# Performance work log

Hardware: AMD Instinct MI355X
Metric: run time of the kernel (lower is better)

Reference implementation:

```python
import jax, jax.numpy as jnp
import numpy as np

N_NODES = 100000
N_EDGES = 1600000
IN_DIM = 128
HEADS = 4
HEAD_DIM = 16  # hidden_dim 64 // 4 heads
HID = HEADS * HEAD_DIM
NEG_SLOPE = 0.2


def setup_inputs() -> dict:
    key = jax.random.key(0)
    ks = jax.random.split(key, 20)
    inp = {
        "x": jax.random.normal(ks[0], (N_NODES, IN_DIM), dtype=jnp.float32),
        "edge_index": jax.random.randint(ks[1], (2, N_EDGES), 0, N_NODES, dtype=jnp.int32),
    }
    dims = [IN_DIM, HID, HID]
    for l in range(3):
        d_in = dims[l]
        sc = 1.0 / np.sqrt(d_in)
        inp[f"w{l}"] = jax.random.normal(ks[2 + 4 * l], (d_in, HID), dtype=jnp.float32) * sc
        inp[f"asrc{l}"] = jax.random.normal(ks[3 + 4 * l], (HEADS, HEAD_DIM), dtype=jnp.float32) * 0.1
        inp[f"adst{l}"] = jax.random.normal(ks[4 + 4 * l], (HEADS, HEAD_DIM), dtype=jnp.float32) * 0.1
        inp[f"b{l}"] = jnp.zeros((HID,), dtype=jnp.float32)
    inp["out_w"] = jax.random.normal(ks[14], (HID, 1), dtype=jnp.float32) * (1.0 / np.sqrt(HID))
    inp["out_b"] = jnp.zeros((1,), dtype=jnp.float32)
    return inp


def _gat_layer(h, src, dst, W, a_src, a_dst, b):
    # h: [N, d_in]; src/dst: [E'] (self-loops already appended)
    n = h.shape[0]
    xh = (h @ W).reshape(n, HEADS, HEAD_DIM)              # [N,H,C]
    al_s = jnp.sum(xh * a_src, axis=-1)                   # [N,H]
    al_d = jnp.sum(xh * a_dst, axis=-1)                   # [N,H]
    e = jax.nn.leaky_relu(al_s[src] + al_d[dst], NEG_SLOPE)  # [E',H]
    # segment-softmax over incoming edges of each destination node
    m = jax.ops.segment_max(e, dst, num_segments=n)       # [N,H]
    p = jnp.exp(e - m[dst])
    z = jax.ops.segment_sum(p, dst, num_segments=n)       # [N,H]
    alpha = p / (z[dst] + 1e-16)                          # [E',H]
    msg = xh[src] * alpha[:, :, None]                     # [E',H,C]
    out = jax.ops.segment_sum(msg, dst, num_segments=n)   # [N,H,C]
    return out.reshape(n, HID) + b


def reference(x, edge_index, w0, asrc0, adst0, b0, w1, asrc1, adst1, b1,
              w2, asrc2, adst2, b2, out_w, out_b):
    n = x.shape[0]
    loops = jnp.arange(n, dtype=edge_index.dtype)
    src = jnp.concatenate([edge_index[0], loops])  # PyG GATConv adds self-loops
    dst = jnp.concatenate([edge_index[1], loops])
    h = x
    params = [(w0, asrc0, adst0, b0), (w1, asrc1, adst1, b1), (w2, asrc2, adst2, b2)]
    for W, a_s, a_d, b in params:
        h = _gat_layer(h, src, dst, W, a_s, a_d, b)
        h = jax.nn.relu(h)
    return (h @ out_w + out_b).squeeze(-1)  # [N]
```

## Files before the change

### kernel.cpp

```cpp
#include <hip/hip_runtime.h>


#define NBMAX 512
#define SCHUNK 4096
#define BCAP 8192
#define PADSLACK 768

typedef __attribute__((ext_vector_type(8))) short bf16x8;
typedef __attribute__((ext_vector_type(4))) float f32x4;

__device__ inline unsigned short bf16_rtn(float x) {
    union { float f; unsigned u; } a; a.f = x;
    return (unsigned short)((a.u + 0x7FFFu + ((a.u >> 16) & 1u)) >> 16);
}
__device__ inline float bf16_to_f(unsigned short s) {
    union { unsigned u; float f; } b; b.u = ((unsigned)s) << 16;
    return b.f;
}

__global__ __launch_bounds__(256) void k_init(int* __restrict__ bhist, int nb,
                                              float* __restrict__ als, float* __restrict__ xh, int n) {
    int i = blockIdx.x * 256 + threadIdx.x;
    if (i < nb) bhist[i] = 0;
    int j = i - NBMAX;
    if (j >= 0 && j < 4) als[(size_t)n * 4 + j] = -1e30f;
    int k = i - NBMAX - 4;
    if (k >= 0 && k < 64) xh[(size_t)n * 64 + k] = 0.f;
}

__global__ __launch_bounds__(256) void k_bhist(const int* __restrict__ dst, int* __restrict__ bhist, int e) {
    __shared__ unsigned int h[NBMAX];
    int t = threadIdx.x;
    h[t] = 0;
    h[t + 256] = 0;
    __syncthreads();
    for (int i = blockIdx.x * 256 + t; i < e; i += gridDim.x * 256)
        atomicAdd(&h[dst[i] >> 8], 1u);
    __syncthreads();
    if (h[t]) atomicAdd(&bhist[t], (int)h[t]);
    if (h[t + 256]) atomicAdd(&bhist[t + 256], (int)h[t + 256]);
}

__global__ __launch_bounds__(512) void k_bscan(const int* __restrict__ bhist, int* __restrict__ boffs,
                                               int* __restrict__ bfill, int nb, int e) {
    __shared__ int s[NBMAX];
    int t = threadIdx.x;
    int v = (t < nb) ? bhist[t] : 0;
    s[t] = v;
    __syncthreads();
    for (int o = 1; o < 512; o <<= 1) {
        int add = (t >= o) ? s[t - o] : 0;
        __syncthreads();
        s[t] += add;
        __syncthreads();
    }
    boffs[t] = s[t] - v;
    if (t == 511) boffs[512] = s[511];
    bfill[t] = 0;
}

__global__ __launch_bounds__(512) void k_bscatter(const int* __restrict__ src, const int* __restrict__ dst,
                                                  const int* __restrict__ boffs, int* __restrict__ bfill,
                                                  unsigned int* __restrict__ edata, int e) {
    __shared__ unsigned int hist[NBMAX];
    __shared__ unsigned int loc[NBMAX];
    __shared__ int gbase[NBMAX];
    __shared__ unsigned int stmp[NBMAX];
    __shared__ unsigned int sortbuf[SCHUNK];
    __shared__ int posbuf[SCHUNK];
    int t = threadIdx.x;
    int i0 = blockIdx.x * SCHUNK;
    int cnt = min(SCHUNK, e - i0);
    hist[t] = 0;
    __syncthreads();
    for (int j = t; j < cnt; j += 512) atomicAdd(&hist[dst[i0 + j] >> 8], 1u);
    __syncthreads();
    unsigned int v = hist[t];
    stmp[t] = v;
    __syncthreads();
    for (int o = 1; o < 512; o <<= 1) {
        unsigned int add = (t >= o) ? stmp[t - o] : 0;
        __syncthreads();
        stmp[t] += add;
        __syncthreads();
    }
    loc[t] = stmp[t] - v;
    int gb = 0;
    if (v > 0) gb = atomicAdd(&bfill[t], (int)v);
    gbase[t] = boffs[t] + gb - (int)loc[t];
    hist[t] = loc[t];
    __syncthreads();
    for (int j = t; j < cnt; j += 512) {
        int d = dst[i0 + j];
        int s = src[i0 + j];
        int b = d >> 8;
        unsigned int p = atomicAdd(&hist[b], 1u);
        sortbuf[p] = (unsigned int)s | ((unsigned int)(d & 255) << 24);
        posbuf[p] = gbase[b] + (int)p;
    }
    __syncthreads();
    for (int j = t; j < cnt; j += 512) edata[posbuf[j]] = sortbuf[j];
}

__global__ __launch_bounds__(256) void k_bfinal(const unsigned int* __restrict__ edata,
                                                const int* __restrict__ boffs, int* __restrict__ poffs,
                                                int* __restrict__ pend, int* __restrict__ ssrc,
                                                int n, int nb) {
    __shared__ unsigned int hist[256];
    __shared__ unsigned int stmp[256];
    __shared__ unsigned int loc[256];
    __shared__ unsigned int cnt_s[256];
    __shared__ unsigned int srcbuf[BCAP];
    int b = blockIdx.x;
    int t = threadIdx.x;
    int e0 = boffs[b], e1 = boffs[b + 1];
    int cnt = e1 - e0;
    int pb = e0 + b * PADSLACK;
    hist[t] = 0;
    __syncthreads();
    for (int j = t; j < cnt; j += 256) atomicAdd(&hist[edata[e0 + j] >> 24], 1u);
    __syncthreads();
    unsigned int v = hist[t];
    unsigned int v4 = (v + 3u) & ~3u;
    cnt_s[t] = v;
    stmp[t] = v4;
    __syncthreads();
    for (int o = 1; o < 256; o <<= 1) {
        unsigned int add = (t >= o) ? stmp[t - o] : 0;
        __syncthreads();
        stmp[t] += add;
        __syncthreads();
    }
    loc[t] = stmp[t] - v4;
    int ptot = (int)stmp[255];
    int node = b * 256 + t;
    if (node < n) {
        poffs[node] = pb + (int)loc[t];
        pend[node] = pb + (int)(loc[t] + v4);
    }
    hist[t] = loc[t];
    __syncthreads();
    if (cnt + PADSLACK <= BCAP) {
        for (int j = t; j < cnt; j += 256) {
            unsigned int p = edata[e0 + j];
            unsigned int pos = atomicAdd(&hist[p >> 24], 1u);
            srcbuf[pos] = p & 0xFFFFFFu;
        }
        for (unsigned int k = v; k < v4; ++k) srcbuf[loc[t] + k] = (unsigned int)n;
        __syncthreads();
        for (int j = t; j < ptot; j += 256) ssrc[pb + j] = (int)srcbuf[j];
    } else {
        for (int j = t; j < cnt; j += 256) {
            unsigned int p = edata[e0 + j];
            unsigned int pos = atomicAdd(&hist[p >> 24], 1u);
            ssrc[pb + (int)pos] = (int)(p & 0xFFFFFFu);
        }
        for (unsigned int k = v; k < v4; ++k) ssrc[pb + (int)(loc[t] + k)] = n;
    }
}

__global__ __launch_bounds__(256) void k_wprep(const float* __restrict__ w0, const float* __restrict__ w1,
                                               const float* __restrict__ w2,
                                               unsigned short* __restrict__ p0h, unsigned short* __restrict__ p0l,
                                               unsigned short* __restrict__ p1h, unsigned short* __restrict__ p1l,
                                               unsigned short* __restrict__ p2h, unsigned short* __restrict__ p2l) {
    int g = blockIdx.x * 256 + threadIdx.x;
    const float* W;
    unsigned short *ph, *pl;
    int idx;
    if (g < 1024) { W = w0; ph = p0h; pl = p0l; idx = g; }
    else if (g < 1536) { W = w1; ph = p1h; pl = p1l; idx = g - 1024; }
    else if (g < 2048) { W = w2; ph = p2h; pl = p2l; idx = g - 1536; }
    else return;
    int ko = idx >> 6, nn = idx & 63;
#pragma unroll
    for (int j = 0; j < 8; ++j) {
        float w = W[(size_t)(ko * 8 + j) * 64 + nn];
        unsigned short hb = bf16_rtn(w);
        ph[(size_t)idx * 8 + j] = hb;
        pl[(size_t)idx * 8 + j] = bf16_rtn(w - bf16_to_f(hb));
    }
}

template <int D_IN>
__global__ __launch_bounds__(256) void k_mgemm(const float* __restrict__ h,
                                               const unsigned short* __restrict__ wph,
                                               const unsigned short* __restrict__ wpl,
                                               const float* __restrict__ asrc, const float* __restrict__ adst,
                                               float* __restrict__ xh, float* __restrict__ als,
                                               float* __restrict__ ald, int n) {
    int t = threadIdx.x;
    int wv = t >> 6, lane = t & 63;
    int quad = lane >> 4, l16 = lane & 15;
    int m0 = blockIdx.x * 64 + wv * 16;
    int node_a = m0 + l16;
    int mm = min(node_a, n - 1);
    const float* hrow = h + (size_t)mm * D_IN + quad * 8;

    f32x4 acc[4];
#pragma unroll
    for (int i = 0; i < 4; ++i) acc[i] = (f32x4){0.f, 0.f, 0.f, 0.f};

    constexpr int KSTEPS = D_IN / 32;
#pragma unroll
    for (int s = 0; s < KSTEPS; ++s) {
        float4 a0 = *(const float4*)(hrow + s * 32);
        float4 a1 = *(const float4*)(hrow + s * 32 + 4);
        float av[8] = {a0.x, a0.y, a0.z, a0.w, a1.x, a1.y, a1.z, a1.w};
        bf16x8 ahi, alo;
#pragma unroll
        for (int j = 0; j < 8; ++j) {
            unsigned short hb = bf16_rtn(av[j]);
            ahi[j] = (short)hb;
            alo[j] = (short)bf16_rtn(av[j] - bf16_to_f(hb));
        }
        const unsigned short* bbase = wph + ((size_t)((s * 4 + quad) * 64 + l16)) * 8;
        const unsigned short* bbasel = wpl + ((size_t)((s * 4 + quad) * 64 + l16)) * 8;
#pragma unroll
        for (int nt = 0; nt < 4; ++nt) {
            bf16x8 bhi = *(const bf16x8*)(bbase + (size_t)nt * 16 * 8);
            bf16x8 blo = *(const bf16x8*)(bbasel + (size_t)nt * 16 * 8);
            acc[nt] = __builtin_amdgcn_mfma_f32_16x16x32_bf16(ahi, bhi, acc[nt], 0, 0, 0);
            acc[nt] = __builtin_amdgcn_mfma_f32_16x16x32_bf16(ahi, blo, acc[nt], 0, 0, 0);
            acc[nt] = __builtin_amdgcn_mfma_f32_16x16x32_bf16(alo, bhi, acc[nt], 0, 0, 0);
        }
    }
#pragma unroll
    for (int nt = 0; nt < 4; ++nt) {
        float as_l = asrc[nt * 16 + l16];
        float ad_l = adst[nt * 16 + l16];
#pragma unroll
        for (int r = 0; r < 4; ++r) {
            int node = m0 + quad * 4 + r;
            float c = acc[nt][r];
            if (node < n) xh[(size_t)node * 64 + nt * 16 + l16] = c;
            float ps = c * as_l, pd = c * ad_l;
            ps += __shfl_xor(ps, 1, 64); pd += __shfl_xor(pd, 1, 64);
            ps += __shfl_xor(ps, 2, 64); pd += __shfl_xor(pd, 2, 64);
            ps += __shfl_xor(ps, 4, 64); pd += __shfl_xor(pd, 4, 64);
            ps += __shfl_xor(ps, 8, 64); pd += __shfl_xor(pd, 8, 64);
            if (l16 == 0 && node < n) {
                als[node * 4 + nt] = ps;
                ald[node * 4 + nt] = pd;
            }
        }
    }
}

__device__ inline float4 lrelu4(float4 v) {
    float4 r;
    r.x = v.x >= 0.f ? v.x : 0.2f * v.x;
    r.y = v.y >= 0.f ? v.y : 0.2f * v.y;
    r.z = v.z >= 0.f ? v.z : 0.2f * v.z;
    r.w = v.w >= 0.f ? v.w : 0.2f * v.w;
    return r;
}

#define ACCUM(LO, HI, ACC, ZS)                                                  \
    {                                                                           \
        int g_ = ((LO) - s0) >> 2, gb_ = ((HI) - s0) >> 2;                      \
        for (; g_ + 4 <= gb_; g_ += 4) {                                        \
            int4 uu0 = *(const int4*)&ub[g_ * 4];                               \
            int4 uu1 = *(const int4*)&ub[g_ * 4 + 4];                           \
            int4 uu2 = *(const int4*)&ub[g_ * 4 + 8];                           \
            int4 uu3 = *(const int4*)&ub[g_ * 4 + 12];                          \
            float4 pp0 = *(const float4*)&per[g_ * 4];                          \
            float4 pp1 = *(const float4*)&per[g_ * 4 + 4];                      \
            float4 pp2 = *(const float4*)&per[g_ * 4 + 8];                      \
            float4 pp3 = *(const float4*)&per[g_ * 4 + 12];                     \
            float x0 = *(const float*)(xl + (size_t)(unsigned)uu0.x);           \
            float x1 = *(const float*)(xl + (size_t)(unsigned)uu0.y);           \
            float x2 = *(const float*)(xl + (size_t)(unsigned)uu0.z);           \
            float x3 = *(const float*)(xl + (size_t)(unsigned)uu0.w);           \
            float x4 = *(const float*)(xl + (size_t)(unsigned)uu1.x);           \
            float x5 = *(const float*)(xl + (size_t)(unsigned)uu1.y);           \
            float x6 = *(const float*)(xl + (size_t)(unsigned)uu1.z);           \
            float x7 = *(const float*)(xl + (size_t)(unsigned)uu1.w);           \
            float x8 = *(const float*)(xl + (size_t)(unsigned)uu2.x);           \
            float x9 = *(const float*)(xl + (size_t)(unsigned)uu2.y);           \
            float xa = *(const float*)(xl + (size_t)(unsigned)uu2.z);           \
            float xb = *(const float*)(xl + (size_t)(unsigned)uu2.w);           \
            float xc = *(const float*)(xl + (size_t)(unsigned)uu3.x);           \
            float xd = *(const float*)(xl + (size_t)(unsigned)uu3.y);           \
            float xe = *(const float*)(xl + (size_t)(unsigned)uu3.z);           \
            float xf = *(const float*)(xl + (size_t)(unsigned)uu3.w);           \
            ZS += pp0.x + pp0.y + pp0.z + pp0.w;                                \
            ZS += pp1.x + pp1.y + pp1.z + pp1.w;                                \
            ZS += pp2.x + pp2.y + pp2.z + pp2.w;                                \
            ZS += pp3.x + pp3.y + pp3.z + pp3.w;                                \
            ACC += pp0.x * x0; ACC += pp0.y * x1; ACC += pp0.z * x2; ACC += pp0.w * x3; \
            ACC += pp1.x * x4; ACC += pp1.y * x5; ACC += pp1.z * x6; ACC += pp1.w * x7; \
            ACC += pp2.x * x8; ACC += pp2.y * x9; ACC += pp2.z * xa; ACC += pp2.w * xb; \
            ACC += pp3.x * xc; ACC += pp3.y * xd; ACC += pp3.z * xe; ACC += pp3.w * xf; \
        }                                                                       \
        for (; g_ < gb_; ++g_) {                                                \
            int4 uu = *(const int4*)&ub[g_ * 4];                                \
            float4 pp = *(const float4*)&per[g_ * 4];                           \
            float x0 = *(const float*)(xl + (size_t)(unsigned)uu.x);            \
            float x1 = *(const float*)(xl + (size_t)(unsigned)uu.y);            \
            float x2 = *(const float*)(xl + (size_t)(unsigned)uu.z);            \
            float x3 = *(const float*)(xl + (size_t)(unsigned)uu.w);            \
            ZS += pp.x + pp.y + pp.z + pp.w;                                    \
            ACC += pp.x * x0; ACC += pp.y * x1; ACC += pp.z * x2; ACC += pp.w * x3; \
        }                                                                       \
    }

__global__ __launch_bounds__(256) void k_agg(const float* __restrict__ xh,
                                             const float* __restrict__ als, const float* __restrict__ ald,
                                             const int* __restrict__ poffs, const int* __restrict__ pend,
                                             const int* __restrict__ ssrc,
                                             const float* __restrict__ bias, float* __restrict__ hout,
                                             const float* __restrict__ outw, const float* __restrict__ outb,
                                             float* __restrict__ fout, int n) {
    __shared__ int s_u[4][64];
    __shared__ float s_pe[4][4][64];
    int wslot = threadIdx.x >> 6;
    int lane = threadIdx.x & 63;
    int w = (blockIdx.x * 256 + threadIdx.x) >> 6;
    int v0 = w << 2;
    if (v0 >= n) return;
    int head = lane >> 4;
    int* ub = s_u[wslot];
    float* per = s_pe[wslot][head];
    float* pew = &s_pe[wslot][0][lane];

    int vlast = n - 1;
    int last = min(v0 + 3, vlast);
    int4 rr = *(const int4*)(poffs + v0);
    int e3 = pend[last];
    int r0 = rr.x;
    int r1 = (v0 + 1 <= last) ? rr.y : e3;
    int r2 = (v0 + 2 <= last) ? rr.z : e3;
    int r3 = (v0 + 3 <= last) ? rr.w : e3;

    const char* xl = (const char*)(xh + lane);
    float acc0 = *(const float*)(xl + ((size_t)(unsigned)v0 << 8));
    float acc1 = *(const float*)(xl + ((size_t)(unsigned)min(v0 + 1, vlast) << 8));
    float acc2 = *(const float*)(xl + ((size_t)(unsigned)min(v0 + 2, vlast) << 8));
    float acc3 = *(const float*)(xl + ((size_t)(unsigned)min(v0 + 3, vlast) << 8));
    float zs0 = 0.f, zs1 = 0.f, zs2 = 0.f, zs3 = 0.f;

    for (int s0 = r0; s0 < e3; s0 += 64) {
        int cnt = min(64, e3 - s0);
        int e = s0 + lane;
        int u = n;
        if (lane < cnt) u = ssrc[e];
        int nid = v0 + (e >= r1) + (e >= r2) + (e >= r3);
        nid = min(nid, vlast);
        float4 alsd = *(const float4*)(als + 4 * (size_t)nid);
        float4 aldd = *(const float4*)(ald + 4 * (size_t)nid);
        float4 m4 = lrelu4(make_float4(alsd.x + aldd.x, alsd.y + aldd.y,
                                       alsd.z + aldd.z, alsd.w + aldd.w));
        float4 alu = *(const float4*)(als + 4 * (size_t)u);
        float4 e4 = lrelu4(make_float4(alu.x + aldd.x, alu.y + aldd.y,
                                       alu.z + aldd.z, alu.w + aldd.w));
        float4 pe;
        pe.x = __expf(e4.x - m4.x);
        pe.y = __expf(e4.y - m4.y);
        pe.z = __expf(e4.z - m4.z);
        pe.w = __expf(e4.w - m4.w);
        ub[lane] = u << 8;
        pew[0] = pe.x;
        pew[64] = pe.y;
        pew[128] = pe.z;
        pew[192] = pe.w;
        int lim = s0 + cnt;
        int hi0 = min(r1, lim);
        int lo1 = max(r1, s0), hi1 = min(r2, lim);
        int lo2 = max(r2, s0), hi2 = min(r3, lim);
        int lo3 = max(r3, s0);
        ACCUM(s0, hi0, acc0, zs0);
        ACCUM(lo1, hi1, acc1, zs1);
        ACCUM(lo2, hi2, acc2, zs2);
        ACCUM(lo3, lim, acc3, zs3);
    }

    float bl = bias[lane];
    float z0 = 1.f + zs0, z1 = 1.f + zs1, z2 = 1.f + zs2, z3 = 1.f + zs3;
    float o0 = fmaxf(acc0 / (z0 + 1e-16f) + bl, 0.f);
    float o1 = fmaxf(acc1 / (z1 + 1e-16f) + bl, 0.f);
    float o2 = fmaxf(acc2 / (z2 + 1e-16f) + bl, 0.f);
    float o3 = fmaxf(acc3 / (z3 + 1e-16f) + bl, 0.f);
    if (outw) {
        float ow = outw[lane];
        float ob = outb[0];
        float t0 = o0 * ow, t1 = o1 * ow, t2 = o2 * ow, t3 = o3 * ow;
#pragma unroll
        for (int d = 32; d; d >>= 1) {
            t0 += __shfl_down(t0, d, 64);
            t1 += __shfl_down(t1, d, 64);
            t2 += __shfl_down(t2, d, 64);
            t3 += __shfl_down(t3, d, 64);
        }
        if (lane == 0) {
            fout[v0] = t0 + ob;
            if (v0 + 1 < n) fout[v0 + 1] = t1 + ob;
            if (v0 + 2 < n) fout[v0 + 2] = t2 + ob;
            if (v0 + 3 < n) fout[v0 + 3] = t3 + ob;
        }
    } else {
        hout[((size_t)v0 << 6) + lane] = o0;
        if (v0 + 1 < n) hout[((size_t)(v0 + 1) << 6) + lane] = o1;
        if (v0 + 2 < n) hout[((size_t)(v0 + 2) << 6) + lane] = o2;
        if (v0 + 3 < n) hout[((size_t)(v0 + 3) << 6) + lane] = o3;
    }
}

extern "C" void kernel_launch(void* const* d_in, const int* in_sizes, int n_in,
                              void* d_out, int out_size, void* d_ws, size_t ws_size,
                              hipStream_t stream) {
    const float* x = (const float*)d_in[0];
    const int* ei = (const int*)d_in[1];
    const float* w[3] = {(const float*)d_in[2], (const float*)d_in[6], (const float*)d_in[10]};
    const float* as[3] = {(const float*)d_in[3], (const float*)d_in[7], (const float*)d_in[11]};
    const float* ad[3] = {(const float*)d_in[4], (const float*)d_in[8], (const float*)d_in[12]};
    const float* b[3] = {(const float*)d_in[5], (const float*)d_in[9], (const float*)d_in[13]};
    const float* outw = (const float*)d_in[14];
    const float* outb = (const float*)d_in[15];

    const int N = in_sizes[0] / 128;
    const int E = in_sizes[1] / 2;
    const int* src = ei;
    const int* dst = ei + E;
    const int NB = (N + 255) / 256;

    char* ws = (char*)d_ws;
    auto alloc = [&](size_t bytes) -> void* {
        void* p = (void*)ws;
        ws += (bytes + 255) & ~(size_t)255;
        return p;
    };
    int* bhist = (int*)alloc(NBMAX * 4);
    int* boffs = (int*)alloc((NBMAX + 1) * 4);
    int* bfill = (int*)alloc(NBMAX * 4);
    int* poffs = (int*)alloc((size_t)(N + 8) * 4);
    int* pend = (int*)alloc((size_t)N * 4);
    int* ssrc = (int*)alloc((size_t)(E + NBMAX * PADSLACK + 256) * 4);
    float* xh = (float*)alloc((size_t)(N + 1) * 64 * 4);
    float* hbuf = (float*)alloc((size_t)N * 64 * 4);
    float* als = (float*)alloc((size_t)(N + 1) * 4 * 4);
    float* ald = (float*)alloc((size_t)N * 4 * 4);
    unsigned short* p0h = (unsigned short*)alloc(8192 * 2);
    unsigned short* p0l = (unsigned short*)alloc(8192 * 2);
    unsigned short* p1h = (unsigned short*)alloc(4096 * 2);
    unsigned short* p1l = (unsigned short*)alloc(4096 * 2);
    unsigned short* p2h = (unsigned short*)alloc(4096 * 2);
    unsigned short* p2l = (unsigned short*)alloc(4096 * 2);
    unsigned int* edata = (unsigned int*)xh;

    k_wprep<<<8, 256, 0, stream>>>(w[0], w[1], w[2], p0h, p0l, p1h, p1l, p2h, p2l);
    k_init<<<3, 256, 0, stream>>>(bhist, NBMAX, als, xh, N);
    k_bhist<<<256, 256, 0, stream>>>(dst, bhist, E);
    k_bscan<<<1, 512, 0, stream>>>(bhist, boffs, bfill, NB, E);
    k_bscatter<<<(E + SCHUNK - 1) / SCHUNK, 512, 0, stream>>>(src, dst, boffs, bfill, edata, E);
    k_bfinal<<<NB, 256, 0, stream>>>(edata, boffs, poffs, pend, ssrc, N, NB);

    const int gblocks = (N + 63) / 64;
    const int ablocks = (N + 15) / 16;

    k_mgemm<128><<<gblocks, 256, 0, stream>>>(x, p0h, p0l, as[0], ad[0], xh, als, ald, N);
    k_agg<<<ablocks, 256, 0, stream>>>(xh, als, ald, poffs, pend, ssrc, b[0], hbuf, nullptr, nullptr, nullptr, N);
    k_mgemm<64><<<gblocks, 256, 0, stream>>>(hbuf, p1h, p1l, as[1], ad[1], xh, als, ald, N);
    k_agg<<<ablocks, 256, 0, stream>>>(xh, als, ald, poffs, pend, ssrc, b[1], hbuf, nullptr, nullptr, nullptr, N);
    k_mgemm<64><<<gblocks, 256, 0, stream>>>(hbuf, p2h, p2l, as[2], ad[2], xh, als, ald, N);
    k_agg<<<ablocks, 256, 0, stream>>>(xh, als, ald, poffs, pend, ssrc, b[2], nullptr, outw, outb, (float*)d_out, N);
}
```

Measured before the change: 434.3 us.

## Prefetch next edge chunk in aggregation, precompute softmax shift, split accumulators

The aggregation loop now software-pipelines its gathers: the next 64-edge chunk's source index, source attention logits, destination logits and softmax shift are loaded before the current chunk is accumulated, hiding gather latency. The per-node softmax shift (leaky_relu of the self-loop score) is computed once in the GEMM kernel and stored in a new mvec buffer, which replaces one gather and the extra arithmetic per edge. Each node's accumulator is split into two independent chains to shorten FMA dependency chains. It costs extra registers, which may lower occupancy, plus an extra N×4 float write and read per layer.

```diff
diff --git a/kernel.cpp b/kernel.cpp
--- a/kernel.cpp
+++ b/kernel.cpp
@@ -109,7 +109,6 @@
     __shared__ unsigned int hist[256];
     __shared__ unsigned int stmp[256];
     __shared__ unsigned int loc[256];
-    __shared__ unsigned int cnt_s[256];
     __shared__ unsigned int srcbuf[BCAP];
     int b = blockIdx.x;
     int t = threadIdx.x;
@@ -122,7 +121,6 @@
     __syncthreads();
     unsigned int v = hist[t];
     unsigned int v4 = (v + 3u) & ~3u;
-    cnt_s[t] = v;
     stmp[t] = v4;
     __syncthreads();
     for (int o = 1; o < 256; o <<= 1) {
@@ -188,7 +186,7 @@
                                                const unsigned short* __restrict__ wpl,
                                                const float* __restrict__ asrc, const float* __restrict__ adst,
                                                float* __restrict__ xh, float* __restrict__ als,
-                                               float* __restrict__ ald, int n) {
+                                               float* __restrict__ ald, float* __restrict__ mvec, int n) {
     int t = threadIdx.x;
     int wv = t >> 6, lane = t & 63;
     int quad = lane >> 4, l16 = lane & 15;
@@ -242,6 +240,8 @@
             if (l16 == 0 && node < n) {
                 als[node * 4 + nt] = ps;
                 ald[node * 4 + nt] = pd;
+                float sm = ps + pd;
+                mvec[node * 4 + nt] = sm >= 0.f ? sm : 0.2f * sm;
             }
         }
     }
@@ -256,7 +256,7 @@
     return r;
 }
 
-#define ACCUM(LO, HI, ACC, ZS)                                                  \
+#define ACCUM(LO, HI, ACCA, ACCB, ZS)                                           \
     {                                                                           \
         int g_ = ((LO) - s0) >> 2, gb_ = ((HI) - s0) >> 2;                      \
         for (; g_ + 4 <= gb_; g_ += 4) {                                        \
@@ -288,10 +288,14 @@
             ZS += pp1.x + pp1.y + pp1.z + pp1.w;                                \
             ZS += pp2.x + pp2.y + pp2.z + pp2.w;                                \
             ZS += pp3.x + pp3.y + pp3.z + pp3.w;                                \
-            ACC += pp0.x * x0; ACC += pp0.y * x1; ACC += pp0.z * x2; ACC += pp0.w * x3; \
-            ACC += pp1.x * x4; ACC += pp1.y * x5; ACC += pp1.z * x6; ACC += pp1.w * x7; \
-            ACC += pp2.x * x8; ACC += pp2.y * x9; ACC += pp2.z * xa; ACC += pp2.w * xb; \
-            ACC += pp3.x * xc; ACC += pp3.y * xd; ACC += pp3.z * xe; ACC += pp3.w * xf; \
+            ACCA += pp0.x * x0; ACCB += pp0.y * x1;                             \
+            ACCA += pp0.z * x2; ACCB += pp0.w * x3;                             \
+            ACCA += pp1.x * x4; ACCB += pp1.y * x5;                             \
+            ACCA += pp1.z * x6; ACCB += pp1.w * x7;                             \
+            ACCA += pp2.x * x8; ACCB += pp2.y * x9;                             \
+            ACCA += pp2.z * xa; ACCB += pp2.w * xb;                             \
+            ACCA += pp3.x * xc; ACCB += pp3.y * xd;                             \
+            ACCA += pp3.z * xe; ACCB += pp3.w * xf;                             \
         }                                                                       \
         for (; g_ < gb_; ++g_) {                                                \
             int4 uu = *(const int4*)&ub[g_ * 4];                                \
@@ -301,12 +305,14 @@
             float x2 = *(const float*)(xl + (size_t)(unsigned)uu.z);            \
             float x3 = *(const float*)(xl + (size_t)(unsigned)uu.w);            \
             ZS += pp.x + pp.y + pp.z + pp.w;                                    \
-            ACC += pp.x * x0; ACC += pp.y * x1; ACC += pp.z * x2; ACC += pp.w * x3; \
+            ACCA += pp.x * x0; ACCB += pp.y * x1;                               \
+            ACCA += pp.z * x2; ACCB += pp.w * x3;                               \
         }                                                                       \
     }
 
 __global__ __launch_bounds__(256) void k_agg(const float* __restrict__ xh,
                                              const float* __restrict__ als, const float* __restrict__ ald,
+                                             const float* __restrict__ mvec,
                                              const int* __restrict__ poffs, const int* __restrict__ pend,
                                              const int* __restrict__ ssrc,
                                              const float* __restrict__ bias, float* __restrict__ hout,
@@ -334,53 +340,65 @@
     int r3 = (v0 + 3 <= last) ? rr.w : e3;
 
     const char* xl = (const char*)(xh + lane);
-    float acc0 = *(const float*)(xl + ((size_t)(unsigned)v0 << 8));
-    float acc1 = *(const float*)(xl + ((size_t)(unsigned)min(v0 + 1, vlast) << 8));
-    float acc2 = *(const float*)(xl + ((size_t)(unsigned)min(v0 + 2, vlast) << 8));
-    float acc3 = *(const float*)(xl + ((size_t)(unsigned)min(v0 + 3, vlast) << 8));
+    float acc0a = *(const float*)(xl + ((size_t)(unsigned)v0 << 8));
+    float acc1a = *(const float*)(xl + ((size_t)(unsigned)min(v0 + 1, vlast) << 8));
+    float acc2a = *(const float*)(xl + ((size_t)(unsigned)min(v0 + 2, vlast) << 8));
+    float acc3a = *(const float*)(xl + ((size_t)(unsigned)min(v0 + 3, vlast) << 8));
+    float acc0b = 0.f, acc1b = 0.f, acc2b = 0.f, acc3b = 0.f;
     float zs0 = 0.f, zs1 = 0.f, zs2 = 0.f, zs3 = 0.f;
 
-    for (int s0 = r0; s0 < e3; s0 += 64) {
+    int s0 = r0;
+    int u_n = n;
+    if (s0 < e3) {
+        if (lane < e3 - s0) u_n = ssrc[s0 + lane];
+    }
+    float4 alu_n = *(const float4*)(als + 4 * (size_t)u_n);
+    int e_n = s0 + lane;
+    int nid_n = min(v0 + (e_n >= r1) + (e_n >= r2) + (e_n >= r3), vlast);
+    float4 ald_n = *(const float4*)(ald + 4 * (size_t)nid_n);
+    float4 m_n = *(const float4*)(mvec + 4 * (size_t)nid_n);
+
+    while (s0 < e3) {
         int cnt = min(64, e3 - s0);
-        int e = s0 + lane;
-        int u = n;
-        if (lane < cnt) u = ssrc[e];
-        int nid = v0 + (e >= r1) + (e >= r2) + (e >= r3);
-        nid = min(nid, vlast);
-        float4 alsd = *(const float4*)(als + 4 * (size_t)nid);
-        float4 aldd = *(const float4*)(ald + 4 * (size_t)nid);
-        float4 m4 = lrelu4(make_float4(alsd.x + aldd.x, alsd.y + aldd.y,
-                                       alsd.z + aldd.z, alsd.w + aldd.w));
-        float4 alu = *(const float4*)(als + 4 * (size_t)u);
-        float4 e4 = lrelu4(make_float4(alu.x + aldd.x, alu.y + aldd.y,
-                                       alu.z + aldd.z, alu.w + aldd.w));
+        float4 e4 = lrelu4(make_float4(alu_n.x + ald_n.x, alu_n.y + ald_n.y,
+                                       alu_n.z + ald_n.z, alu_n.w + ald_n.w));
         float4 pe;
-        pe.x = __expf(e4.x - m4.x);
-        pe.y = __expf(e4.y - m4.y);
-        pe.z = __expf(e4.z - m4.z);
-        pe.w = __expf(e4.w - m4.w);
-        ub[lane] = u << 8;
+        pe.x = __expf(e4.x - m_n.x);
+        pe.y = __expf(e4.y - m_n.y);
+        pe.z = __expf(e4.z - m_n.z);
+        pe.w = __expf(e4.w - m_n.w);
+        ub[lane] = u_n << 8;
         pew[0] = pe.x;
         pew[64] = pe.y;
         pew[128] = pe.z;
         pew[192] = pe.w;
+        int s1 = s0 + 64;
+        if (s1 < e3) {
+            u_n = n;
+            if (lane < e3 - s1) u_n = ssrc[s1 + lane];
+            alu_n = *(const float4*)(als + 4 * (size_t)u_n);
+            int e1 = s1 + lane;
+            int nid1 = min(v0 + (e1 >= r1) + (e1 >= r2) + (e1 >= r3), vlast);
+            ald_n = *(const float4*)(ald + 4 * (size_t)nid1);
+            m_n = *(const float4*)(mvec + 4 * (size_t)nid1);
+        }
         int lim = s0 + cnt;
         int hi0 = min(r1, lim);
         int lo1 = max(r1, s0), hi1 = min(r2, lim);
         int lo2 = max(r2, s0), hi2 = min(r3, lim);
         int lo3 = max(r3, s0);
-        ACCUM(s0, hi0, acc0, zs0);
-        ACCUM(lo1, hi1, acc1, zs1);
-        ACCUM(lo2, hi2, acc2, zs2);
-        ACCUM(lo3, lim, acc3, zs3);
+        ACCUM(s0, hi0, acc0a, acc0b, zs0);
+        ACCUM(lo1, hi1, acc1a, acc1b, zs1);
+        ACCUM(lo2, hi2, acc2a, acc2b, zs2);
+        ACCUM(lo3, lim, acc3a, acc3b, zs3);
+        s0 = s1;
     }
 
     float bl = bias[lane];
-    float z0 = 1.f + zs0, z1 = 1.f + zs1, z2 = 1.f + zs2, z3 = 1.f + zs3;
-    float o0 = fmaxf(acc0 / (z0 + 1e-16f) + bl, 0.f);
-    float o1 = fmaxf(acc1 / (z1 + 1e-16f) + bl, 0.f);
-    float o2 = fmaxf(acc2 / (z2 + 1e-16f) + bl, 0.f);
-    float o3 = fmaxf(acc3 / (z3 + 1e-16f) + bl, 0.f);
+    float o0 = fmaxf((acc0a + acc0b) / (1.f + zs0 + 1e-16f) + bl, 0.f);
+    float o1 = fmaxf((acc1a + acc1b) / (1.f + zs1 + 1e-16f) + bl, 0.f);
+    float o2 = fmaxf((acc2a + acc2b) / (1.f + zs2 + 1e-16f) + bl, 0.f);
+    float o3 = fmaxf((acc3a + acc3b) / (1.f + zs3 + 1e-16f) + bl, 0.f);
     if (outw) {
         float ow = outw[lane];
         float ob = outb[0];
@@ -440,6 +458,7 @@
     float* hbuf = (float*)alloc((size_t)N * 64 * 4);
     float* als = (float*)alloc((size_t)(N + 1) * 4 * 4);
     float* ald = (float*)alloc((size_t)N * 4 * 4);
+    float* mvec = (float*)alloc((size_t)N * 4 * 4);
     unsigned short* p0h = (unsigned short*)alloc(8192 * 2);
     unsigned short* p0l = (unsigned short*)alloc(8192 * 2);
     unsigned short* p1h = (unsigned short*)alloc(4096 * 2);
@@ -458,10 +477,10 @@
     const int gblocks = (N + 63) / 64;
     const int ablocks = (N + 15) / 16;
 
-    k_mgemm<128><<<gblocks, 256, 0, stream>>>(x, p0h, p0l, as[0], ad[0], xh, als, ald, N);
-    k_agg<<<ablocks, 256, 0, stream>>>(xh, als, ald, poffs, pend, ssrc, b[0], hbuf, nullptr, nullptr, nullptr, N);
-    k_mgemm<64><<<gblocks, 256, 0, stream>>>(hbuf, p1h, p1l, as[1], ad[1], xh, als, ald, N);
-    k_agg<<<ablocks, 256, 0, stream>>>(xh, als, ald, poffs, pend, ssrc, b[1], hbuf, nullptr, nullptr, nullptr, N);
-    k_mgemm<64><<<gblocks, 256, 0, stream>>>(hbuf, p2h, p2l, as[2], ad[2], xh, als, ald, N);
-    k_agg<<<ablocks, 256, 0, stream>>>(xh, als, ald, poffs, pend, ssrc, b[2], nullptr, outw, outb, (float*)d_out, N);
-}
+    k_mgemm<128><<<gblocks, 256, 0, stream>>>(x, p0h, p0l, as[0], ad[0], xh, als, ald, mvec, N);
+    k_agg<<<ablocks, 256, 0, stream>>>(xh, als, ald, mvec, poffs, pend, ssrc, b[0], hbuf, nullptr, nullptr, nullptr, N);
+    k_mgemm<64><<<gblocks, 256, 0, stream>>>(hbuf, p1h, p1l, as[1], ad[1], xh, als, ald, mvec, N);
+    k_agg<<<ablocks, 256, 0, stream>>>(xh, als, ald, mvec, poffs, pend, ssrc, b[1], hbuf, nullptr, nullptr, nullptr, N);
+    k_mgemm<64><<<gblocks, 256, 0, stream>>>(hbuf, p2h, p2l, as[2], ad[2], xh, als, ald, mvec, N);
+    k_agg<<<ablocks, 256, 0, stream>>>(xh, als, ald, mvec, poffs, pend, ssrc, b[2], nullptr, outw, outb, (float*)d_out, N);
+}
```

Result: no change. 435.4 us (+0.3%).
